# Performance work log

Measured on AMD Instinct MI355X. Metric: run time of the kernel, lower is better.

## Reference

```python
import jax, jax.numpy as jnp
import numpy as np

KERNEL_MUL = 2.0
KERNEL_NUM = 5


def setup_inputs() -> dict:
    key = jax.random.key(0)
    k1, k2 = jax.random.split(key)
    source = jax.random.normal(k1, (4096, 256), dtype=jnp.float32)
    target = jax.random.normal(k2, (4096, 256), dtype=jnp.float32)
    return {"source": source, "target": target}


def reference(source, target):
    batch_size = source.shape[0]
    total = jnp.concatenate([source, target], axis=0)  # [2N, D]
    n_samples = total.shape[0]
    # avoids the [2N, 2N, D] expand the torch code materializes).
    sq = jnp.sum(total * total, axis=1)  # [2N]
    gram = total @ total.T               # [2N, 2N]
    L2 = sq[:, None] + sq[None, :] - 2.0 * gram
    # bandwidth computed from detached distances (torch uses .data)
    bw = jax.lax.stop_gradient(jnp.sum(L2)) / (n_samples ** 2 - n_samples)
    bw = bw / (KERNEL_MUL ** (KERNEL_NUM // 2))
    kernels = jnp.zeros_like(L2)
    for i in range(KERNEL_NUM):
        kernels = kernels + jnp.exp(-L2 / (bw * (KERNEL_MUL ** i)))
    XY = jnp.mean(kernels[:batch_size, batch_size:])
    YX = jnp.mean(kernels[batch_size:, :batch_size])
    loss = -XY - YX
    return loss
```

## Files before the change

kernel.cpp:

```cpp
#include <hip/hip_runtime.h>
#include <hip/hip_bf16.h>


#define D 256
#define NROWS 4096
#define SQ_OFF 4
#define S1PART 8196
#define CROSSPART 8324
#define COLPART 9348
#define ABF_OFF 42116
#define BBF_OFF 566404
#define WS_NEED_FLOATS 1090692

typedef __attribute__((ext_vector_type(8))) short short8;
typedef __attribute__((ext_vector_type(16))) float float16;
typedef unsigned short ushort_t;

__device__ inline unsigned pack2_bf16(float a, float b) {
  unsigned ua = __float_as_uint(a);
  ua += 0x7FFFu + ((ua >> 16) & 1u);
  unsigned ub = __float_as_uint(b);
  ub += 0x7FFFu + ((ub >> 16) & 1u);
  return (ua >> 16) | (ub & 0xFFFF0000u);
}

__device__ inline void gload_lds16(const ushort_t* g, ushort_t* l) {
  __builtin_amdgcn_global_load_lds(
      (const __attribute__((address_space(1))) unsigned int*)g,
      (__attribute__((address_space(3))) unsigned int*)l, 16, 0, 0);
}

__global__ __launch_bounds__(256) void prep_kernel(const float* __restrict__ src,
                                                   const float* __restrict__ tgt,
                                                   float* __restrict__ ws,
                                                   int writeBf16) {
  __shared__ float csL[4][256];
  __shared__ float s1L[4];
  ushort_t* Abf = (ushort_t*)(ws + ABF_OFF);
  ushort_t* Bbf = (ushort_t*)(ws + BBF_OFF);
  int t = threadIdx.x;
  int wave = t >> 6, lane = t & 63;
  int rowBase = blockIdx.x * 64 + wave * 16;
  float cs0 = 0.f, cs1 = 0.f, cs2 = 0.f, cs3 = 0.f, s1 = 0.f;
  for (int r = 0; r < 16; ++r) {
    int row = rowBase + r;
    int isA = row < NROWS;
    const float* p = isA ? (src + (size_t)row * D) : (tgt + (size_t)(row - NROWS) * D);
    float4 v = reinterpret_cast<const float4*>(p)[lane];
    if (writeBf16) {
      ushort_t* dst = (isA ? Abf + (size_t)row * D : Bbf + (size_t)(row - NROWS) * D) + lane * 4;
      *reinterpret_cast<uint2*>(dst) = make_uint2(pack2_bf16(v.x, v.y), pack2_bf16(v.z, v.w));
    }
    cs0 += v.x; cs1 += v.y; cs2 += v.z; cs3 += v.w;
    float sq = v.x * v.x + v.y * v.y + v.z * v.z + v.w * v.w;
#pragma unroll
    for (int off = 32; off; off >>= 1) sq += __shfl_xor(sq, off, 64);
    if (lane == 0) { ws[SQ_OFF + row] = sq; s1 += sq; }
  }
  csL[wave][lane * 4 + 0] = cs0;
  csL[wave][lane * 4 + 1] = cs1;
  csL[wave][lane * 4 + 2] = cs2;
  csL[wave][lane * 4 + 3] = cs3;
  if (lane == 0) s1L[wave] = s1;
  __syncthreads();
  ws[COLPART + blockIdx.x * 256 + t] = csL[0][t] + csL[1][t] + csL[2][t] + csL[3][t];
  if (t == 0) ws[S1PART + blockIdx.x] = s1L[0] + s1L[1] + s1L[2] + s1L[3];
}

__global__ __launch_bounds__(256) void bw_kernel(float* __restrict__ ws) {
  __shared__ float red[256];
  __shared__ float s1red[128];
  int t = threadIdx.x;
  float colsum = 0.f;
#pragma unroll 8
  for (int b = 0; b < 128; ++b) colsum += ws[COLPART + b * 256 + t];
  red[t] = colsum * colsum;
  if (t < 128) s1red[t] = ws[S1PART + t];
  __syncthreads();
#pragma unroll
  for (int s = 128; s > 0; s >>= 1) {
    if (t < s) red[t] += red[t + s];
    if (s > 1 && t < (s >> 1)) s1red[t] += s1red[t + (s >> 1)];
    __syncthreads();
  }
  if (t == 0) {
    double n = 8192.0;
    double sumL2 = 2.0 * n * (double)s1red[0] - 2.0 * (double)red[0];
    double bw = sumL2 / (n * n - n) / 4.0;
    ws[2] = (float)(-1.4426950408889634 / (16.0 * bw));
  }
}

template <int BF16SRC>
__global__ __launch_bounds__(256) void cross_kernel(const float* __restrict__ A32,
                                                    const float* __restrict__ B32,
                                                    const ushort_t* __restrict__ Abf,
                                                    const ushort_t* __restrict__ Bbf,
                                                    float* __restrict__ ws) {
  __shared__ ushort_t Abuf[128 * 64];
  __shared__ ushort_t Bbuf[128 * 64];
  __shared__ float sqAs[128], sqBs[128];
  __shared__ float red[256];
  int t = threadIdx.x;
  int bid = blockIdx.x;
  int xcd = bid & 7, q = bid >> 3;
  int bi = (xcd >> 1) * 8 + (q >> 4);
  int bj = (xcd & 1) * 16 + (q & 15);
  int rowBase = bi * 128, colBase = bj * 128;
  int wave = t >> 6, lane = t & 63;
  int wm = wave >> 1, wn = wave & 1;
  int hi = lane >> 5;
  int lr = lane & 31;
  int sr = t >> 4, sc = t & 15;

  if (t < 128) sqAs[t] = ws[SQ_OFF + rowBase + t];
  else         sqBs[t - 128] = ws[SQ_OFF + NROWS + colBase + (t - 128)];

  float16 acc00, acc01, acc10, acc11;
#pragma unroll
  for (int r = 0; r < 16; ++r) { acc00[r] = 0.f; acc01[r] = 0.f; acc10[r] = 0.f; acc11[r] = 0.f; }

  int lrow8 = lane >> 3;
  int lchunk = (lane & 7) ^ lrow8;
  for (int k0 = 0; k0 < D; k0 += 64) {
    if (BF16SRC) {
      int w32 = wave * 32;
#pragma unroll
      for (int j = 0; j < 4; ++j) {
        int r0 = w32 + j * 8;
        gload_lds16(Abf + (size_t)(rowBase + r0 + lrow8) * D + k0 + (lchunk << 3),
                    &Abuf[r0 * 64]);
        gload_lds16(Bbf + (size_t)(colBase + r0 + lrow8) * D + k0 + (lchunk << 3),
                    &Bbuf[r0 * 64]);
      }
    } else {
#pragma unroll
      for (int i = 0; i < 8; ++i) {
        int r = sr + 16 * i;
        int swz = (sc * 4) ^ ((r & 7) << 3);
        float4 va = *reinterpret_cast<const float4*>(&A32[(size_t)(rowBase + r) * D + k0 + sc * 4]);
        *reinterpret_cast<uint2*>(&Abuf[r * 64 + swz]) =
            make_uint2(pack2_bf16(va.x, va.y), pack2_bf16(va.z, va.w));
        float4 vb = *reinterpret_cast<const float4*>(&B32[(size_t)(colBase + r) * D + k0 + sc * 4]);
        *reinterpret_cast<uint2*>(&Bbuf[r * 64 + swz]) =
            make_uint2(pack2_bf16(vb.x, vb.y), pack2_bf16(vb.z, vb.w));
      }
    }
    __syncthreads();
#pragma unroll
    for (int ks = 0; ks < 4; ++ks) {
      int c0 = ks * 2 + hi;
      int ra0 = wm * 64 + lr, ra1 = ra0 + 32;
      int rb0 = wn * 64 + lr, rb1 = rb0 + 32;
      short8 a0 = *reinterpret_cast<const short8*>(&Abuf[ra0 * 64 + ((c0 ^ (ra0 & 7)) << 3)]);
      short8 a1 = *reinterpret_cast<const short8*>(&Abuf[ra1 * 64 + ((c0 ^ (ra1 & 7)) << 3)]);
      short8 b0 = *reinterpret_cast<const short8*>(&Bbuf[rb0 * 64 + ((c0 ^ (rb0 & 7)) << 3)]);
      short8 b1 = *reinterpret_cast<const short8*>(&Bbuf[rb1 * 64 + ((c0 ^ (rb1 & 7)) << 3)]);
      acc00 = __builtin_amdgcn_mfma_f32_32x32x16_bf16(a0, b0, acc00, 0, 0, 0);
      acc01 = __builtin_amdgcn_mfma_f32_32x32x16_bf16(a0, b1, acc01, 0, 0, 0);
      acc10 = __builtin_amdgcn_mfma_f32_32x32x16_bf16(a1, b0, acc10, 0, 0, 0);
      acc11 = __builtin_amdgcn_mfma_f32_32x32x16_bf16(a1, b1, acc11, 0, 0, 0);
    }
    __syncthreads();
  }

  float c2 = ws[2];
  float local = 0.f;
#pragma unroll
  for (int m2 = 0; m2 < 2; ++m2) {
#pragma unroll
    for (int n2 = 0; n2 < 2; ++n2) {
      const float16& g = (m2 == 0) ? ((n2 == 0) ? acc00 : acc01)
                                   : ((n2 == 0) ? acc10 : acc11);
      float sB = sqBs[wn * 64 + n2 * 32 + lr];
#pragma unroll
      for (int r = 0; r < 16; ++r) {
        int row = (r & 3) + 8 * (r >> 2) + 4 * hi;
        float dd = sqAs[wm * 64 + m2 * 32 + row] + sB - 2.0f * g[r];
        float y = __builtin_amdgcn_exp2f(dd * c2);
        float y2 = y * y, y4 = y2 * y2, y8 = y4 * y4, y16 = y8 * y8;
        local += y + y2 + y4 + y8 + y16;
      }
    }
  }
  red[t] = local;
  __syncthreads();
#pragma unroll
  for (int s = 128; s > 0; s >>= 1) {
    if (t < s) red[t] += red[t + s];
    __syncthreads();
  }
  if (t == 0) ws[CROSSPART + bid] = red[0];
}

__global__ __launch_bounds__(256) void finalize_kernel(const float* __restrict__ ws,
                                                       float* __restrict__ out) {
  __shared__ float red[256];
  int t = threadIdx.x;
  red[t] = ws[CROSSPART + t] + ws[CROSSPART + 256 + t] +
           ws[CROSSPART + 512 + t] + ws[CROSSPART + 768 + t];
  __syncthreads();
#pragma unroll
  for (int s = 128; s > 0; s >>= 1) {
    if (t < s) red[t] += red[t + s];
    __syncthreads();
  }
  if (t == 0) out[0] = -2.0f * (red[0] * (1.0f / 16777216.0f));
}

extern "C" void kernel_launch(void* const* d_in, const int* in_sizes, int n_in,
                              void* d_out, int out_size, void* d_ws, size_t ws_size,
                              hipStream_t stream) {
  const float* src = (const float*)d_in[0];
  const float* tgt = (const float*)d_in[1];
  float* ws = (float*)d_ws;
  float* out = (float*)d_out;
  int useBf16 = ws_size >= (size_t)WS_NEED_FLOATS * sizeof(float);
  const ushort_t* Abf = (const ushort_t*)(ws + ABF_OFF);
  const ushort_t* Bbf = (const ushort_t*)(ws + BBF_OFF);

  prep_kernel<<<128, 256, 0, stream>>>(src, tgt, ws, useBf16);
  bw_kernel<<<1, 256, 0, stream>>>(ws);
  if (useBf16)
    cross_kernel<1><<<1024, 256, 0, stream>>>(src, tgt, Abf, Bbf, ws);
  else
    cross_kernel<0><<<1024, 256, 0, stream>>>(src, tgt, Abf, Bbf, ws);
  finalize_kernel<<<1, 256, 0, stream>>>(ws, out);
}
```

Measured before the change: 94.79 us.

## Enlarge cross tile to 256x256 with 512 threads and double-buffered LDS staging

```diff
diff --git a/kernel.cpp b/kernel.cpp
--- a/kernel.cpp
+++ b/kernel.cpp
@@ -92,113 +92,131 @@
 }
 
 template <int BF16SRC>
-__global__ __launch_bounds__(256) void cross_kernel(const float* __restrict__ A32,
-                                                    const float* __restrict__ B32,
-                                                    const ushort_t* __restrict__ Abf,
-                                                    const ushort_t* __restrict__ Bbf,
-                                                    float* __restrict__ ws) {
-  __shared__ ushort_t Abuf[128 * 64];
-  __shared__ ushort_t Bbuf[128 * 64];
-  __shared__ float sqAs[128], sqBs[128];
-  __shared__ float red[256];
+__global__ __launch_bounds__(512, 2) void cross_kernel(const float* __restrict__ A32,
+                                                       const float* __restrict__ B32,
+                                                       const ushort_t* __restrict__ Abf,
+                                                       const ushort_t* __restrict__ Bbf,
+                                                       float* __restrict__ ws) {
+  __shared__ ushort_t Ab[2][256 * 64];
+  __shared__ ushort_t Bb[2][256 * 64];
+  __shared__ float sqAs[256], sqBs[256];
+  __shared__ float red[8];
   int t = threadIdx.x;
   int bid = blockIdx.x;
-  int xcd = bid & 7, q = bid >> 3;
-  int bi = (xcd >> 1) * 8 + (q >> 4);
-  int bj = (xcd & 1) * 16 + (q & 15);
-  int rowBase = bi * 128, colBase = bj * 128;
+  int xcd = bid & 7, idx = bid >> 3;
+  int bi = (xcd >> 1) * 4 + (idx >> 3);
+  int bj = (xcd & 1) * 8 + (idx & 7);
+  int rowBase = bi * 256, colBase = bj * 256;
   int wave = t >> 6, lane = t & 63;
-  int wm = wave >> 1, wn = wave & 1;
-  int hi = lane >> 5;
-  int lr = lane & 31;
-  int sr = t >> 4, sc = t & 15;
-
-  if (t < 128) sqAs[t] = ws[SQ_OFF + rowBase + t];
-  else         sqBs[t - 128] = ws[SQ_OFF + NROWS + colBase + (t - 128)];
-
-  float16 acc00, acc01, acc10, acc11;
-#pragma unroll
-  for (int r = 0; r < 16; ++r) { acc00[r] = 0.f; acc01[r] = 0.f; acc10[r] = 0.f; acc11[r] = 0.f; }
-
-  int lrow8 = lane >> 3;
-  int lchunk = (lane & 7) ^ lrow8;
-  for (int k0 = 0; k0 < D; k0 += 64) {
+  int wm = wave >> 2, wn = wave & 3;
+  int hi = lane >> 5, lr = lane & 31;
+
+  if (t < 256) sqAs[t] = ws[SQ_OFF + rowBase + t];
+  else         sqBs[t - 256] = ws[SQ_OFF + NROWS + colBase + (t - 256)];
+
+  float16 acc[4][2];
+#pragma unroll
+  for (int i = 0; i < 4; ++i)
+#pragma unroll
+    for (int j = 0; j < 2; ++j)
+#pragma unroll
+      for (int r = 0; r < 16; ++r) acc[i][j][r] = 0.f;
+
+  int grow = lane >> 3;
+  int gchunk = (lane & 7) ^ grow;
+
+  auto STAGE = [&](int buf, int k0) {
     if (BF16SRC) {
-      int w32 = wave * 32;
 #pragma unroll
       for (int j = 0; j < 4; ++j) {
-        int r0 = w32 + j * 8;
-        gload_lds16(Abf + (size_t)(rowBase + r0 + lrow8) * D + k0 + (lchunk << 3),
-                    &Abuf[r0 * 64]);
-        gload_lds16(Bbf + (size_t)(colBase + r0 + lrow8) * D + k0 + (lchunk << 3),
-                    &Bbuf[r0 * 64]);
+        int r0 = (wave * 4 + j) * 8;
+        gload_lds16(Abf + (size_t)(rowBase + r0 + grow) * D + k0 + gchunk * 8, &Ab[buf][r0 * 64]);
+        gload_lds16(Bbf + (size_t)(colBase + r0 + grow) * D + k0 + gchunk * 8, &Bb[buf][r0 * 64]);
       }
     } else {
 #pragma unroll
-      for (int i = 0; i < 8; ++i) {
-        int r = sr + 16 * i;
-        int swz = (sc * 4) ^ ((r & 7) << 3);
-        float4 va = *reinterpret_cast<const float4*>(&A32[(size_t)(rowBase + r) * D + k0 + sc * 4]);
-        *reinterpret_cast<uint2*>(&Abuf[r * 64 + swz]) =
-            make_uint2(pack2_bf16(va.x, va.y), pack2_bf16(va.z, va.w));
-        float4 vb = *reinterpret_cast<const float4*>(&B32[(size_t)(colBase + r) * D + k0 + sc * 4]);
-        *reinterpret_cast<uint2*>(&Bbuf[r * 64 + swz]) =
-            make_uint2(pack2_bf16(vb.x, vb.y), pack2_bf16(vb.z, vb.w));
+      for (int i = 0; i < 4; ++i) {
+        int r = (t >> 3) + 64 * i;
+        int s = t & 7;
+        int slot = (s ^ (r & 7)) << 3;
+        const float* pa = &A32[(size_t)(rowBase + r) * D + k0 + s * 8];
+        float4 a0 = *reinterpret_cast<const float4*>(pa);
+        float4 a1 = *reinterpret_cast<const float4*>(pa + 4);
+        *reinterpret_cast<uint4*>(&Ab[buf][r * 64 + slot]) =
+            make_uint4(pack2_bf16(a0.x, a0.y), pack2_bf16(a0.z, a0.w),
+                       pack2_bf16(a1.x, a1.y), pack2_bf16(a1.z, a1.w));
+        const float* pb = &B32[(size_t)(colBase + r) * D + k0 + s * 8];
+        float4 b0 = *reinterpret_cast<const float4*>(pb);
+        float4 b1 = *reinterpret_cast<const float4*>(pb + 4);
+        *reinterpret_cast<uint4*>(&Bb[buf][r * 64 + slot]) =
+            make_uint4(pack2_bf16(b0.x, b0.y), pack2_bf16(b0.z, b0.w),
+                       pack2_bf16(b1.x, b1.y), pack2_bf16(b1.z, b1.w));
       }
     }
-    __syncthreads();
+  };
+
+  auto COMPUTE = [&](int buf) {
 #pragma unroll
     for (int ks = 0; ks < 4; ++ks) {
-      int c0 = ks * 2 + hi;
-      int ra0 = wm * 64 + lr, ra1 = ra0 + 32;
-      int rb0 = wn * 64 + lr, rb1 = rb0 + 32;
-      short8 a0 = *reinterpret_cast<const short8*>(&Abuf[ra0 * 64 + ((c0 ^ (ra0 & 7)) << 3)]);
-      short8 a1 = *reinterpret_cast<const short8*>(&Abuf[ra1 * 64 + ((c0 ^ (ra1 & 7)) << 3)]);
-      short8 b0 = *reinterpret_cast<const short8*>(&Bbuf[rb0 * 64 + ((c0 ^ (rb0 & 7)) << 3)]);
-      short8 b1 = *reinterpret_cast<const short8*>(&Bbuf[rb1 * 64 + ((c0 ^ (rb1 & 7)) << 3)]);
-      acc00 = __builtin_amdgcn_mfma_f32_32x32x16_bf16(a0, b0, acc00, 0, 0, 0);
-      acc01 = __builtin_amdgcn_mfma_f32_32x32x16_bf16(a0, b1, acc01, 0, 0, 0);
-      acc10 = __builtin_amdgcn_mfma_f32_32x32x16_bf16(a1, b0, acc10, 0, 0, 0);
-      acc11 = __builtin_amdgcn_mfma_f32_32x32x16_bf16(a1, b1, acc11, 0, 0, 0);
-    }
+      int off = ((ks * 2 + hi) ^ (lr & 7)) << 3;
+      short8 af[4], bf[2];
+#pragma unroll
+      for (int fr = 0; fr < 4; ++fr)
+        af[fr] = *reinterpret_cast<const short8*>(&Ab[buf][(wm * 128 + fr * 32 + lr) * 64 + off]);
+#pragma unroll
+      for (int fc = 0; fc < 2; ++fc)
+        bf[fc] = *reinterpret_cast<const short8*>(&Bb[buf][(wn * 64 + fc * 32 + lr) * 64 + off]);
+#pragma unroll
+      for (int fr = 0; fr < 4; ++fr)
+#pragma unroll
+        for (int fc = 0; fc < 2; ++fc)
+          acc[fr][fc] = __builtin_amdgcn_mfma_f32_32x32x16_bf16(af[fr], bf[fc], acc[fr][fc], 0, 0, 0);
+    }
+  };
+
+  STAGE(0, 0);
+  __syncthreads();
+#pragma unroll
+  for (int step = 0; step < 4; ++step) {
+    if (step < 3) STAGE((step + 1) & 1, (step + 1) * 64);
+    COMPUTE(step & 1);
     __syncthreads();
   }
 
   float c2 = ws[2];
   float local = 0.f;
 #pragma unroll
-  for (int m2 = 0; m2 < 2; ++m2) {
-#pragma unroll
-    for (int n2 = 0; n2 < 2; ++n2) {
-      const float16& g = (m2 == 0) ? ((n2 == 0) ? acc00 : acc01)
-                                   : ((n2 == 0) ? acc10 : acc11);
-      float sB = sqBs[wn * 64 + n2 * 32 + lr];
+  for (int fr = 0; fr < 4; ++fr) {
+#pragma unroll
+    for (int fc = 0; fc < 2; ++fc) {
+      float sB = sqBs[wn * 64 + fc * 32 + lr];
 #pragma unroll
       for (int r = 0; r < 16; ++r) {
-        int row = (r & 3) + 8 * (r >> 2) + 4 * hi;
-        float dd = sqAs[wm * 64 + m2 * 32 + row] + sB - 2.0f * g[r];
+        int rrow = (r & 3) + 8 * (r >> 2) + 4 * hi;
+        float dd = sqAs[wm * 128 + fr * 32 + rrow] + sB - 2.0f * acc[fr][fc][r];
         float y = __builtin_amdgcn_exp2f(dd * c2);
         float y2 = y * y, y4 = y2 * y2, y8 = y4 * y4, y16 = y8 * y8;
         local += y + y2 + y4 + y8 + y16;
       }
     }
   }
-  red[t] = local;
-  __syncthreads();
-#pragma unroll
-  for (int s = 128; s > 0; s >>= 1) {
-    if (t < s) red[t] += red[t + s];
-    __syncthreads();
-  }
-  if (t == 0) ws[CROSSPART + bid] = red[0];
+#pragma unroll
+  for (int off = 32; off; off >>= 1) local += __shfl_xor(local, off, 64);
+  if (lane == 0) red[wave] = local;
+  __syncthreads();
+  if (t == 0) {
+    float s = 0.f;
+#pragma unroll
+    for (int i = 0; i < 8; ++i) s += red[i];
+    ws[CROSSPART + bid] = s;
+  }
 }
 
 __global__ __launch_bounds__(256) void finalize_kernel(const float* __restrict__ ws,
                                                        float* __restrict__ out) {
   __shared__ float red[256];
   int t = threadIdx.x;
-  red[t] = ws[CROSSPART + t] + ws[CROSSPART + 256 + t] +
-           ws[CROSSPART + 512 + t] + ws[CROSSPART + 768 + t];
+  red[t] = ws[CROSSPART + t];
   __syncthreads();
 #pragma unroll
   for (int s = 128; s > 0; s >>= 1) {
@@ -222,8 +240,8 @@
   prep_kernel<<<128, 256, 0, stream>>>(src, tgt, ws, useBf16);
   bw_kernel<<<1, 256, 0, stream>>>(ws);
   if (useBf16)
-    cross_kernel<1><<<1024, 256, 0, stream>>>(src, tgt, Abf, Bbf, ws);
+    cross_kernel<1><<<256, 512, 0, stream>>>(src, tgt, Abf, Bbf, ws);
   else
-    cross_kernel<0><<<1024, 256, 0, stream>>>(src, tgt, Abf, Bbf, ws);
+    cross_kernel<0><<<256, 512, 0, stream>>>(src, tgt, Abf, Bbf, ws);
   finalize_kernel<<<1, 256, 0, stream>>>(ws, out);
 }
```

Result: no change. 96.47 us (+1.8%).
